# Kernel optimization log

Hardware: AMD Instinct MI355X
Metric: run time of the kernel (lower is better)

Reference implementation:

```python
import jax, jax.numpy as jnp
import numpy as np

PATCH_SIZES = [8, 16, 24, 48]
SEQ_LEN = 1440
D_MODEL = 512
C_IN = 14
B = 64
BEFF = B * C_IN  # '(B C)' leading dim, individual=True
EPS = float(np.finfo(np.float64).eps)  # np.finfo(float).eps in the original


def setup_inputs() -> dict:
    key = jax.random.key(0)
    ks = jax.random.split(key, 9)
    inp = {}
    for i, p in enumerate(PATCH_SIZES):
        L = -(-SEQ_LEN // p)  # ceil(seq_len / patch_size)
        inp[f"x{i}"] = jax.random.normal(ks[i], (BEFF, L, D_MODEL), dtype=jnp.float32)
        inp[f"W{i}"] = jax.random.normal(ks[4 + i], (p, D_MODEL), dtype=jnp.float32) * (1.0 / np.sqrt(D_MODEL))
        inp[f"b{i}"] = jnp.zeros((p,), dtype=jnp.float32)
    g = jax.random.uniform(ks[8], (BEFF, len(PATCH_SIZES)), dtype=jnp.float32)
    inp["gates"] = g / jnp.sum(g, axis=1, keepdims=True)  # dense soft gates (all nonzero)
    return inp


def reference(x0, x1, x2, x3, W0, b0, W1, b1, W2, b2, W3, b3, gates):
    xs = [x0, x1, x2, x3]
    Ws = [W0, W1, W2, W3]
    bs = [b0, b1, b2, b3]
    outs = []
    for x, W, b in zip(xs, Ws, bs):
        # per-scale Linear(d_model, patch_size); dropout p=0.0 is identity
        y = jnp.einsum('bld,pd->blp', x, W) + b          # [Beff, L_i, p_i]
        # rearrange 'B L (P C) -> B (L P) C' with C=1, then slice to seq_len
        y = y.reshape(y.shape[0], -1, 1)[:, :SEQ_LEN, :]  # [Beff, S, 1]
        outs.append(y)
    # CrossScalePeriodicFeatureAggregator with dense gates:
    # cat(xs,0).exp(), gate-weighted, index_add over batch == weighted sum over experts
    stacked = jnp.exp(jnp.stack(outs, axis=0))            # [E, Beff, S, 1]
    combined = jnp.einsum('ebsd,be->bsd', stacked, gates)  # [Beff, S, 1]
    combined = jnp.where(combined == 0, EPS, combined)
    combined = jnp.log(combined)
    # rearrange '(B C) L D -> B L (C D)' with C=c_in
    out = combined.reshape(B, C_IN, SEQ_LEN, 1).transpose(0, 2, 1, 3).reshape(B, SEQ_LEN, C_IN)
    return out
```

## Files before the change

### kernel.cpp

```cpp
#include <hip/hip_runtime.h>
#include <hip/hip_bf16.h>

#define SEQ   1440
#define DM    512
#define BEFFN 896
#define CIN   14
#define NBAT  64

typedef unsigned int u32;

__device__ __forceinline__ float bf_lo(u32 u) { union { u32 i; float f; } a; a.i = u << 16;          return a.f; }
__device__ __forceinline__ float bf_hi(u32 u) { union { u32 i; float f; } a; a.i = u & 0xFFFF0000u;  return a.f; }

__global__ void detect_dtype(const void* __restrict__ gates, int* __restrict__ flag)
{
    if (threadIdx.x == 0 && blockIdx.x == 0) {
        const u32* gb = (const u32*)gates;
        float eb = 0.f;
        for (int r = 0; r < 8; ++r) {
            float sb = 0.f;
            for (int k = 0; k < 4; ++k) {
                int idx = r * 4 + k;
                u32 t = gb[idx >> 1];
                sb += (idx & 1) ? bf_hi(t) : bf_lo(t);
            }
            eb += fabsf(sb - 1.f);
        }
        flag[0] = (eb < 0.25f) ? 1 : 0;
    }
}

template<int PO, int P, int L, int RB, int JB, int NACT, int BF>
__device__ __forceinline__ void row_batch(const void* __restrict__ x_,
                                          const void* __restrict__ W_,
                                          const void* __restrict__ b_,
                                          float* __restrict__ ylds, int beff)
{
    int lane = threadIdx.x & 63;
    if (lane >= NACT) return;
    int l = RB + lane;

    float acc[PO];
    if (BF) {
        const u32* bb = (const u32*)b_;
#pragma unroll
        for (int j = 0; j < PO; j += 2) {
            u32 t = bb[(JB + j) >> 1];
            acc[j] = bf_lo(t); acc[j + 1] = bf_hi(t);
        }
    } else {
        const float* bb = (const float*)b_;
#pragma unroll
        for (int j = 0; j < PO; ++j) acc[j] = bb[JB + j];
    }

    if (BF) {
        const uint4* xr = (const uint4*)((const __hip_bfloat16*)x_ + ((long long)beff * L + l) * DM);
        const u32*   Wb = (const u32*)W_;
        for (int d = 0; d < DM; d += 8) {
            uint4 v = xr[d >> 3];
            float xv[8];
            xv[0] = bf_lo(v.x); xv[1] = bf_hi(v.x);
            xv[2] = bf_lo(v.y); xv[3] = bf_hi(v.y);
            xv[4] = bf_lo(v.z); xv[5] = bf_hi(v.z);
            xv[6] = bf_lo(v.w); xv[7] = bf_hi(v.w);
#pragma unroll
            for (int j = 0; j < PO; ++j) {
                const u32* wr = Wb + (((JB + j) * DM + d) >> 1);
                u32 w0 = wr[0], w1 = wr[1], w2 = wr[2], w3 = wr[3];
                acc[j] = fmaf(xv[0], bf_lo(w0), acc[j]);
                acc[j] = fmaf(xv[1], bf_hi(w0), acc[j]);
                acc[j] = fmaf(xv[2], bf_lo(w1), acc[j]);
                acc[j] = fmaf(xv[3], bf_hi(w1), acc[j]);
                acc[j] = fmaf(xv[4], bf_lo(w2), acc[j]);
                acc[j] = fmaf(xv[5], bf_hi(w2), acc[j]);
                acc[j] = fmaf(xv[6], bf_lo(w3), acc[j]);
                acc[j] = fmaf(xv[7], bf_hi(w3), acc[j]);
            }
        }
    } else {
        const float4* xr = (const float4*)((const float*)x_ + ((long long)beff * L + l) * DM);
        const float*  Wf = (const float*)W_;
        for (int d = 0; d < DM; d += 8) {
            float4 a = xr[d >> 2], b = xr[(d >> 2) + 1];
            float xv[8] = { a.x, a.y, a.z, a.w, b.x, b.y, b.z, b.w };
#pragma unroll
            for (int j = 0; j < PO; ++j) {
                const float* wr = Wf + (JB + j) * DM + d;
#pragma unroll
                for (int u = 0; u < 8; ++u) acc[j] = fmaf(xv[u], wr[u], acc[j]);
            }
        }
    }

    float* yo = ylds + l * P + JB;
#pragma unroll
    for (int j = 0; j < PO; j += 4)
        *(float4*)(yo + j) = make_float4(acc[j], acc[j + 1], acc[j + 2], acc[j + 3]);
}

__global__ __launch_bounds__(384) void fused_all(
    const void* __restrict__ x0, const void* __restrict__ x1,
    const void* __restrict__ x2, const void* __restrict__ x3,
    const void* __restrict__ W0, const void* __restrict__ W1,
    const void* __restrict__ W2, const void* __restrict__ W3,
    const void* __restrict__ b0, const void* __restrict__ b1,
    const void* __restrict__ b2, const void* __restrict__ b3,
    const void* __restrict__ gates, void* __restrict__ out,
    const int* __restrict__ flag)
{
    __shared__ float ysh[4 * SEQ];
    const int beff = blockIdx.x;
    const int w = threadIdx.x >> 6;
    const int isbf = flag[0];

    if (isbf) {
        switch (w) {
            case 0: row_batch<24, 24, 60,   0,  0, 60, 1>(x2, W2, b2, ysh + 2 * SEQ, beff); break;
            case 1: row_batch<24, 48, 30,   0,  0, 30, 1>(x3, W3, b3, ysh + 3 * SEQ, beff); break;
            case 2: row_batch<24, 48, 30,   0, 24, 30, 1>(x3, W3, b3, ysh + 3 * SEQ, beff); break;
            case 3: row_batch<16, 16, 90,   0,  0, 64, 1>(x1, W1, b1, ysh + 1 * SEQ, beff);
                    row_batch< 8,  8, 180,  0,  0, 64, 1>(x0, W0, b0, ysh,           beff); break;
            case 4: row_batch<16, 16, 90,  64,  0, 26, 1>(x1, W1, b1, ysh + 1 * SEQ, beff);
                    row_batch< 8,  8, 180, 64,  0, 64, 1>(x0, W0, b0, ysh,           beff); break;
            case 5: row_batch< 8,  8, 180, 128, 0, 52, 1>(x0, W0, b0, ysh,           beff); break;
        }
    } else {
        switch (w) {
            case 0: row_batch<24, 24, 60,   0,  0, 60, 0>(x2, W2, b2, ysh + 2 * SEQ, beff); break;
            case 1: row_batch<24, 48, 30,   0,  0, 30, 0>(x3, W3, b3, ysh + 3 * SEQ, beff); break;
            case 2: row_batch<24, 48, 30,   0, 24, 30, 0>(x3, W3, b3, ysh + 3 * SEQ, beff); break;
            case 3: row_batch<16, 16, 90,   0,  0, 64, 0>(x1, W1, b1, ysh + 1 * SEQ, beff);
                    row_batch< 8,  8, 180,  0,  0, 64, 0>(x0, W0, b0, ysh,           beff); break;
            case 4: row_batch<16, 16, 90,  64,  0, 26, 0>(x1, W1, b1, ysh + 1 * SEQ, beff);
                    row_batch< 8,  8, 180, 64,  0, 64, 0>(x0, W0, b0, ysh,           beff); break;
            case 5: row_batch< 8,  8, 180, 128, 0, 52, 0>(x0, W0, b0, ysh,           beff); break;
        }
    }
    __syncthreads();

    const int Bi = beff / CIN, c = beff % CIN;
    float g0, g1, g2, g3;
    if (isbf) {
        const u32* gg = (const u32*)gates;
        u32 t0 = gg[beff * 2], t1 = gg[beff * 2 + 1];
        g0 = bf_lo(t0); g1 = bf_hi(t0); g2 = bf_lo(t1); g3 = bf_hi(t1);
    } else {
        float4 gv = ((const float4*)gates)[beff];
        g0 = gv.x; g1 = gv.y; g2 = gv.z; g3 = gv.w;
    }

    for (int s = threadIdx.x; s < SEQ; s += 384) {
        float acc = g0 * __expf(ysh[s])
                  + g1 * __expf(ysh[SEQ + s])
                  + g2 * __expf(ysh[2 * SEQ + s])
                  + g3 * __expf(ysh[3 * SEQ + s]);
        if (acc == 0.f) acc = 2.2204460492503131e-16f;
        float r = __logf(acc);
        long long oi = (long long)(Bi * SEQ + s) * CIN + c;
        if (isbf) ((__hip_bfloat16*)out)[oi] = __float2bfloat16(r);
        else      ((float*)out)[oi] = r;
    }
}

extern "C" void kernel_launch(void* const* d_in, const int* in_sizes, int n_in,
                              void* d_out, int out_size, void* d_ws, size_t ws_size,
                              hipStream_t stream)
{
    const void *x[4] = {0,0,0,0}, *W[4] = {0,0,0,0}, *b[4] = {0,0,0,0}, *gates = 0;
    for (int i = 0; i < n_in; ++i) {
        const void* p = d_in[i];
        switch (in_sizes[i]) {
            case 82575360: x[0] = p; break;
            case 41287680: x[1] = p; break;
            case 27525120: x[2] = p; break;
            case 13762560: x[3] = p; break;
            case 4096:  W[0] = p; break;
            case 8192:  W[1] = p; break;
            case 12288: W[2] = p; break;
            case 24576: W[3] = p; break;
            case 8:  b[0] = p; break;
            case 16: b[1] = p; break;
            case 24: b[2] = p; break;
            case 48: b[3] = p; break;
            case 3584: gates = p; break;
        }
    }

    int* flag = (int*)d_ws;

    detect_dtype<<<1, 64, 0, stream>>>(gates, flag);
    fused_all<<<BEFFN, 384, 0, stream>>>(x[0], x[1], x[2], x[3],
                                         W[0], W[1], W[2], W[3],
                                         b[0], b[1], b[2], b[3],
                                         gates, d_out, flag);
}
```

Before: 882.2 us.

## Rebalance per-wave work into uniform 8-output chunks via dispatch table

Replaces the templated per-wave row batches with a 16-entry table of uniform 8-output work items, four per wave, across 256-thread blocks with launch_bounds(256,4). The intent is to balance work across waves, cut register pressure from 24-wide accumulators, and raise occupancy. The x loads are also software-pipelined with double-buffered registers, and the bf16 path uses a packed bf16 dot2 instruction when the builtin is available. Runtime table lookup and a generic function replace compile-time specialization, which may add address arithmetic and mean x rows are re-read once per 8-output chunk.

```diff
diff --git a/kernel.cpp b/kernel.cpp
--- a/kernel.cpp
+++ b/kernel.cpp
@@ -5,12 +5,27 @@
 #define DM    512
 #define BEFFN 896
 #define CIN   14
-#define NBAT  64
 
 typedef unsigned int u32;
 
 __device__ __forceinline__ float bf_lo(u32 u) { union { u32 i; float f; } a; a.i = u << 16;          return a.f; }
 __device__ __forceinline__ float bf_hi(u32 u) { union { u32 i; float f; } a; a.i = u & 0xFFFF0000u;  return a.f; }
+
+#if __has_builtin(__builtin_amdgcn_fdot2_f32_bf16)
+typedef __bf16 bf16x2 __attribute__((ext_vector_type(2)));
+__device__ __forceinline__ float dot2bf(u32 a, u32 b, float c)
+{
+    union { u32 u; bf16x2 v; } ua, ub; ua.u = a; ub.u = b;
+    return __builtin_amdgcn_fdot2_f32_bf16(ua.v, ub.v, c, false);
+}
+#else
+__device__ __forceinline__ float dot2bf(u32 a, u32 b, float c)
+{
+    c = fmaf(bf_lo(a), bf_lo(b), c);
+    c = fmaf(bf_hi(a), bf_hi(b), c);
+    return c;
+}
+#endif
 
 __global__ void detect_dtype(const void* __restrict__ gates, int* __restrict__ flag)
 {
@@ -30,76 +45,112 @@
     }
 }
 
-template<int PO, int P, int L, int RB, int JB, int NACT, int BF>
-__device__ __forceinline__ void row_batch(const void* __restrict__ x_,
+__device__ __forceinline__ void batch_bf(const void* __restrict__ x_,
+                                         const void* __restrict__ W_,
+                                         const void* __restrict__ b_,
+                                         float* __restrict__ ylds, int beff,
+                                         int L, int P, int RB, int JB, int NACT)
+{
+    const int lane = threadIdx.x & 63;
+    if (lane < NACT) {
+        const int l = RB + lane;
+
+        float acc[8];
+        {
+            const u32* bb = (const u32*)b_ + (JB >> 1);
+#pragma unroll
+            for (int j = 0; j < 8; j += 2) { u32 t = bb[j >> 1]; acc[j] = bf_lo(t); acc[j + 1] = bf_hi(t); }
+        }
+
+        const uint4* xr = (const uint4*)((const __hip_bfloat16*)x_ + ((long long)beff * L + l) * DM);
+        const u32*   wp = (const u32*)W_ + ((long long)JB * DM >> 1);
+
+        uint4 va0 = xr[0], va1 = xr[1], va2 = xr[2], va3 = xr[3];
+        uint4 vb0 = xr[4], vb1 = xr[5], vb2 = xr[6], vb3 = xr[7];
+
+#define PQ(vq, qk) do {                                             \
+        _Pragma("unroll")                                           \
+        for (int j = 0; j < 8; ++j) {                               \
+            const u32* wr = wp + j * 256 + (qk) * 4;                \
+            acc[j] = dot2bf((vq).x, wr[0], acc[j]);                 \
+            acc[j] = dot2bf((vq).y, wr[1], acc[j]);                 \
+            acc[j] = dot2bf((vq).z, wr[2], acc[j]);                 \
+            acc[j] = dot2bf((vq).w, wr[3], acc[j]);                 \
+        } } while (0)
+
+#pragma unroll
+        for (int g2 = 0; g2 < 8; ++g2) {
+            PQ(va0, 0); PQ(va1, 1); PQ(va2, 2); PQ(va3, 3);
+            if (g2 < 7) { int q = 8 * (g2 + 1); va0 = xr[q]; va1 = xr[q + 1]; va2 = xr[q + 2]; va3 = xr[q + 3]; }
+            PQ(vb0, 4); PQ(vb1, 5); PQ(vb2, 6); PQ(vb3, 7);
+            if (g2 < 7) { int q = 8 * (g2 + 1); vb0 = xr[q + 4]; vb1 = xr[q + 5]; vb2 = xr[q + 6]; vb3 = xr[q + 7]; }
+            wp += 32;
+        }
+#undef PQ
+
+        float* yo = ylds + l * P + JB;
+        *(float4*)(yo)     = make_float4(acc[0], acc[1], acc[2], acc[3]);
+        *(float4*)(yo + 4) = make_float4(acc[4], acc[5], acc[6], acc[7]);
+    }
+}
+
+__device__ __forceinline__ void batch_f32(const void* __restrict__ x_,
                                           const void* __restrict__ W_,
                                           const void* __restrict__ b_,
-                                          float* __restrict__ ylds, int beff)
-{
-    int lane = threadIdx.x & 63;
-    if (lane >= NACT) return;
-    int l = RB + lane;
-
-    float acc[PO];
-    if (BF) {
-        const u32* bb = (const u32*)b_;
-#pragma unroll
-        for (int j = 0; j < PO; j += 2) {
-            u32 t = bb[(JB + j) >> 1];
-            acc[j] = bf_lo(t); acc[j + 1] = bf_hi(t);
-        }
-    } else {
-        const float* bb = (const float*)b_;
-#pragma unroll
-        for (int j = 0; j < PO; ++j) acc[j] = bb[JB + j];
-    }
-
-    if (BF) {
-        const uint4* xr = (const uint4*)((const __hip_bfloat16*)x_ + ((long long)beff * L + l) * DM);
-        const u32*   Wb = (const u32*)W_;
-        for (int d = 0; d < DM; d += 8) {
-            uint4 v = xr[d >> 3];
-            float xv[8];
-            xv[0] = bf_lo(v.x); xv[1] = bf_hi(v.x);
-            xv[2] = bf_lo(v.y); xv[3] = bf_hi(v.y);
-            xv[4] = bf_lo(v.z); xv[5] = bf_hi(v.z);
-            xv[6] = bf_lo(v.w); xv[7] = bf_hi(v.w);
-#pragma unroll
-            for (int j = 0; j < PO; ++j) {
-                const u32* wr = Wb + (((JB + j) * DM + d) >> 1);
-                u32 w0 = wr[0], w1 = wr[1], w2 = wr[2], w3 = wr[3];
-                acc[j] = fmaf(xv[0], bf_lo(w0), acc[j]);
-                acc[j] = fmaf(xv[1], bf_hi(w0), acc[j]);
-                acc[j] = fmaf(xv[2], bf_lo(w1), acc[j]);
-                acc[j] = fmaf(xv[3], bf_hi(w1), acc[j]);
-                acc[j] = fmaf(xv[4], bf_lo(w2), acc[j]);
-                acc[j] = fmaf(xv[5], bf_hi(w2), acc[j]);
-                acc[j] = fmaf(xv[6], bf_lo(w3), acc[j]);
-                acc[j] = fmaf(xv[7], bf_hi(w3), acc[j]);
-            }
-        }
-    } else {
+                                          float* __restrict__ ylds, int beff,
+                                          int L, int P, int RB, int JB, int NACT)
+{
+    const int lane = threadIdx.x & 63;
+    if (lane < NACT) {
+        const int l = RB + lane;
+
+        float acc[8];
+        {
+            const float* bb = (const float*)b_ + JB;
+#pragma unroll
+            for (int j = 0; j < 8; ++j) acc[j] = bb[j];
+        }
+
         const float4* xr = (const float4*)((const float*)x_ + ((long long)beff * L + l) * DM);
-        const float*  Wf = (const float*)W_;
-        for (int d = 0; d < DM; d += 8) {
-            float4 a = xr[d >> 2], b = xr[(d >> 2) + 1];
-            float xv[8] = { a.x, a.y, a.z, a.w, b.x, b.y, b.z, b.w };
-#pragma unroll
-            for (int j = 0; j < PO; ++j) {
-                const float* wr = Wf + (JB + j) * DM + d;
-#pragma unroll
-                for (int u = 0; u < 8; ++u) acc[j] = fmaf(xv[u], wr[u], acc[j]);
-            }
-        }
-    }
-
-    float* yo = ylds + l * P + JB;
-#pragma unroll
-    for (int j = 0; j < PO; j += 4)
-        *(float4*)(yo + j) = make_float4(acc[j], acc[j + 1], acc[j + 2], acc[j + 3]);
-}
-
-__global__ __launch_bounds__(384) void fused_all(
+        const float*  wp = (const float*)W_ + (long long)JB * DM;
+
+        float4 va0 = xr[0], va1 = xr[1], va2 = xr[2], va3 = xr[3];
+        float4 vb0 = xr[4], vb1 = xr[5], vb2 = xr[6], vb3 = xr[7];
+
+#define PQF(vq, qk) do {                                            \
+        _Pragma("unroll")                                           \
+        for (int j = 0; j < 8; ++j) {                               \
+            const float* wr = wp + j * 512 + (qk) * 4;              \
+            acc[j] = fmaf((vq).x, wr[0], acc[j]);                   \
+            acc[j] = fmaf((vq).y, wr[1], acc[j]);                   \
+            acc[j] = fmaf((vq).z, wr[2], acc[j]);                   \
+            acc[j] = fmaf((vq).w, wr[3], acc[j]);                   \
+        } } while (0)
+
+#pragma unroll
+        for (int g2 = 0; g2 < 16; ++g2) {
+            PQF(va0, 0); PQF(va1, 1); PQF(va2, 2); PQF(va3, 3);
+            if (g2 < 15) { int q = 8 * (g2 + 1); va0 = xr[q]; va1 = xr[q + 1]; va2 = xr[q + 2]; va3 = xr[q + 3]; }
+            PQF(vb0, 4); PQF(vb1, 5); PQF(vb2, 6); PQF(vb3, 7);
+            if (g2 < 15) { int q = 8 * (g2 + 1); vb0 = xr[q + 4]; vb1 = xr[q + 5]; vb2 = xr[q + 6]; vb3 = xr[q + 7]; }
+            wp += 32;
+        }
+#undef PQF
+
+        float* yo = ylds + l * P + JB;
+        *(float4*)(yo)     = make_float4(acc[0], acc[1], acc[2], acc[3]);
+        *(float4*)(yo + 4) = make_float4(acc[4], acc[5], acc[6], acc[7]);
+    }
+}
+
+__device__ const int dtab[16][6] = {
+    {0, 180,  8,   0,  0, 64}, {0, 180,  8,  64,  0, 64}, {0, 180,  8, 128,  0, 52}, {1,  90, 16,   0,  0, 64},
+    {1,  90, 16,  64,  0, 26}, {1,  90, 16,   0,  8, 64}, {1,  90, 16,  64,  8, 26}, {2,  60, 24,   0,  0, 60},
+    {2,  60, 24,   0,  8, 60}, {2,  60, 24,   0, 16, 60}, {3,  30, 48,   0,  0, 30}, {3,  30, 48,   0,  8, 30},
+    {3,  30, 48,   0, 16, 30}, {3,  30, 48,   0, 24, 30}, {3,  30, 48,   0, 32, 30}, {3,  30, 48,   0, 40, 30},
+};
+
+__global__ __launch_bounds__(256, 4) void fused_all(
     const void* __restrict__ x0, const void* __restrict__ x1,
     const void* __restrict__ x2, const void* __restrict__ x3,
     const void* __restrict__ W0, const void* __restrict__ W1,
@@ -114,28 +165,17 @@
     const int w = threadIdx.x >> 6;
     const int isbf = flag[0];
 
-    if (isbf) {
-        switch (w) {
-            case 0: row_batch<24, 24, 60,   0,  0, 60, 1>(x2, W2, b2, ysh + 2 * SEQ, beff); break;
-            case 1: row_batch<24, 48, 30,   0,  0, 30, 1>(x3, W3, b3, ysh + 3 * SEQ, beff); break;
-            case 2: row_batch<24, 48, 30,   0, 24, 30, 1>(x3, W3, b3, ysh + 3 * SEQ, beff); break;
-            case 3: row_batch<16, 16, 90,   0,  0, 64, 1>(x1, W1, b1, ysh + 1 * SEQ, beff);
-                    row_batch< 8,  8, 180,  0,  0, 64, 1>(x0, W0, b0, ysh,           beff); break;
-            case 4: row_batch<16, 16, 90,  64,  0, 26, 1>(x1, W1, b1, ysh + 1 * SEQ, beff);
-                    row_batch< 8,  8, 180, 64,  0, 64, 1>(x0, W0, b0, ysh,           beff); break;
-            case 5: row_batch< 8,  8, 180, 128, 0, 52, 1>(x0, W0, b0, ysh,           beff); break;
-        }
-    } else {
-        switch (w) {
-            case 0: row_batch<24, 24, 60,   0,  0, 60, 0>(x2, W2, b2, ysh + 2 * SEQ, beff); break;
-            case 1: row_batch<24, 48, 30,   0,  0, 30, 0>(x3, W3, b3, ysh + 3 * SEQ, beff); break;
-            case 2: row_batch<24, 48, 30,   0, 24, 30, 0>(x3, W3, b3, ysh + 3 * SEQ, beff); break;
-            case 3: row_batch<16, 16, 90,   0,  0, 64, 0>(x1, W1, b1, ysh + 1 * SEQ, beff);
-                    row_batch< 8,  8, 180,  0,  0, 64, 0>(x0, W0, b0, ysh,           beff); break;
-            case 4: row_batch<16, 16, 90,  64,  0, 26, 0>(x1, W1, b1, ysh + 1 * SEQ, beff);
-                    row_batch< 8,  8, 180, 64,  0, 64, 0>(x0, W0, b0, ysh,           beff); break;
-            case 5: row_batch< 8,  8, 180, 128, 0, 52, 0>(x0, W0, b0, ysh,           beff); break;
-        }
+#pragma unroll 1
+    for (int bi = 0; bi < 4; ++bi) {
+        const int e  = __builtin_amdgcn_readfirstlane(w * 4 + bi);
+        const int sc = dtab[e][0], L = dtab[e][1], P  = dtab[e][2];
+        const int RB = dtab[e][3], JB = dtab[e][4], NA = dtab[e][5];
+        const void* xp = sc == 0 ? x0 : sc == 1 ? x1 : sc == 2 ? x2 : x3;
+        const void* Wp = sc == 0 ? W0 : sc == 1 ? W1 : sc == 2 ? W2 : W3;
+        const void* bp = sc == 0 ? b0 : sc == 1 ? b1 : sc == 2 ? b2 : b3;
+        float* yl = ysh + sc * SEQ;
+        if (isbf) batch_bf (xp, Wp, bp, yl, beff, L, P, RB, JB, NA);
+        else      batch_f32(xp, Wp, bp, yl, beff, L, P, RB, JB, NA);
     }
     __syncthreads();
 
@@ -150,7 +190,7 @@
         g0 = gv.x; g1 = gv.y; g2 = gv.z; g3 = gv.w;
     }
 
-    for (int s = threadIdx.x; s < SEQ; s += 384) {
+    for (int s = threadIdx.x; s < SEQ; s += 256) {
         float acc = g0 * __expf(ysh[s])
                   + g1 * __expf(ysh[SEQ + s])
                   + g2 * __expf(ysh[2 * SEQ + s])
@@ -190,7 +230,7 @@
     int* flag = (int*)d_ws;
 
     detect_dtype<<<1, 64, 0, stream>>>(gates, flag);
-    fused_all<<<BEFFN, 384, 0, stream>>>(x[0], x[1], x[2], x[3],
+    fused_all<<<BEFFN, 256, 0, stream>>>(x[0], x[1], x[2], x[3],
                                          W[0], W[1], W[2], W[3],
                                          b[0], b[1], b[2], b[3],
                                          gates, d_out, flag);
```

Result: slower. 904.1 us (+2.5%).
